# Kernel optimization log

Measured on AMD Instinct MI355X. Metric: run time of the kernel, lower is better.

The kernel has to match this reference:

```python
import jax, jax.numpy as jnp
import numpy as np

B, N, D, H, QK, HID = 4, 1024, 1024, 16, 64, 4096
BETA = 1.0 / float(np.sqrt(QK))  # default attn_beta = 1/sqrt(qk_dim)


def setup_inputs() -> dict:
    key = jax.random.key(0)
    k1, k2, k3, k4 = jax.random.split(key, 4)
    x = jax.random.normal(k1, (B, N, D), dtype=jnp.float32)
    scale = 1.0 / float(np.sqrt(D))
    Wq = jax.random.normal(k2, (H, QK, D), dtype=jnp.float32) * scale
    Wk = jax.random.normal(k3, (H, QK, D), dtype=jnp.float32) * scale
    W_hop = jax.random.normal(k4, (D, HID), dtype=jnp.float32) * scale
    return {"x": x, "Wq": Wq, "Wk": Wk, "W_hop": W_hop}


def _energy(x, Wq, Wk, W_hop):
    # Graph energy attention (dense path, no adjacency / mask)
    q = jnp.einsum('bnd,hqd->bhnq', x, Wq)  # [B,H,N,QK]
    k = jnp.einsum('bnd,hqd->bhnq', x, Wk)  # [B,H,N,QK]
    scores = BETA * jnp.einsum('bhnq,bhmq->bhnm', q, k)  # [B,H,N,N]
    e_attn = -(1.0 / BETA) * jnp.sum(jax.nn.logsumexp(scores, axis=-1))
    # Hopfield energy: -1/2 * sum relu(x W)^2
    h = jax.nn.relu(jnp.einsum('bnd,de->bne', x, W_hop))  # [B,N,HID]
    e_hop = -0.5 * jnp.sum(h * h)
    return e_attn + e_hop


def reference(x, Wq, Wk, W_hop):
    # Module returns (grad of energy w.r.t. x, energy) via grad_and_value
    energy, grad = jax.value_and_grad(_energy, argnums=0)(x, Wq, Wk, W_hop)
    return grad, energy
```

## Files before the change

### kernel.cpp

```cpp
#include <hip/hip_runtime.h>
#include <hip/hip_bf16.h>
#include <math.h>

#define BETA 0.125f
#define INV_BETA 8.0f

typedef __attribute__((ext_vector_type(8))) short short8v;
typedef __attribute__((ext_vector_type(4))) float f32x4;
typedef union { short8v v; unsigned short u[8]; } v8u;

#define OFF_XB   0u
#define OFF_WCB  2097152u
#define OFF_WCTB 3145728u
#define OFF_WHB  4194304u
#define OFF_WHTB 6291456u
#define OFF_H    8388608u
#define OFF_QB   16777216u
#define OFF_KB   18874368u
#define OFF_QT   20971520u
#define OFF_KT   23068672u
#define OFF_DQK  25165824u
#define OFF_LSE  29360128u
#define OFF_PL   29425664u
#define OFF_PH   29429760u

__device__ __forceinline__ unsigned short f2b(float f) {
    unsigned u = __float_as_uint(f);
    return (unsigned short)((u + 0x7fffu + ((u >> 16) & 1u)) >> 16);
}

__device__ __forceinline__ void gload_lds16(const unsigned short* g, void* l) {
    __builtin_amdgcn_global_load_lds(
        (const __attribute__((address_space(1))) unsigned int*)g,
        (__attribute__((address_space(3))) unsigned int*)l, 16, 0, 0);
}

__global__ __launch_bounds__(256) void k_castall(const float* __restrict__ x,
                                                 const float* __restrict__ Wq,
                                                 const float* __restrict__ Wk,
                                                 const float* __restrict__ Whop,
                                                 unsigned short* __restrict__ XB,
                                                 unsigned short* __restrict__ WCB,
                                                 unsigned short* __restrict__ WHB) {
    int i = blockIdx.x * 256 + threadIdx.x;
    const float* s;
    unsigned short* d;
    int j;
    if (i < 1048576) { s = x; d = XB; j = i; }
    else if (i < 1310720) { s = Wq; d = WCB; j = i - 1048576; }
    else if (i < 1572864) { s = Wk; d = WCB + 1048576; j = i - 1310720; }
    else { s = Whop; d = WHB; j = i - 1572864; }
    float4 v = ((const float4*)s)[j];
    ushort4 o;
    o.x = f2b(v.x); o.y = f2b(v.y); o.z = f2b(v.z); o.w = f2b(v.w);
    ((ushort4*)d)[j] = o;
}

__global__ void k_tall(const float* __restrict__ Wq, const float* __restrict__ Wk,
                       const float* __restrict__ Whop,
                       unsigned short* __restrict__ WCTB, unsigned short* __restrict__ WHTB) {
    __shared__ float t[32][33];
    int bx = blockIdx.x;
    int tx = threadIdx.x, ty = threadIdx.y;
    if (bx < 64) {
        int j0 = bx * 32, d0 = blockIdx.y * 32;
#pragma unroll
        for (int i = 0; i < 4; ++i) {
            int j = j0 + ty + 8 * i;
            const float* src = (j < 1024) ? (Wq + (size_t)j * 1024) : (Wk + (size_t)(j - 1024) * 1024);
            t[ty + 8 * i][tx] = src[d0 + tx];
        }
        __syncthreads();
#pragma unroll
        for (int i = 0; i < 4; ++i)
            WCTB[(size_t)(d0 + ty + 8 * i) * 2048 + j0 + tx] = f2b(t[tx][ty + 8 * i]);
    } else {
        int e0 = (bx - 64) * 32, d0 = blockIdx.y * 32;
#pragma unroll
        for (int i = 0; i < 4; ++i)
            t[ty + 8 * i][tx] = Whop[(size_t)(d0 + ty + 8 * i) * 4096 + e0 + tx];
        __syncthreads();
#pragma unroll
        for (int i = 0; i < 4; ++i)
            WHTB[(size_t)(e0 + ty + 8 * i) * 1024 + d0 + tx] = f2b(t[tx][ty + 8 * i]);
    }
}

template <int MI, int NJ>
__device__ __forceinline__ void gemm_core(const unsigned short* __restrict__ A, int lda,
                                          const unsigned short* __restrict__ Bm, int ldb,
                                          int kdim, int rowBase, int colBase,
                                          unsigned short* ldsA, unsigned short* ldsB,
                                          f32x4 (&acc)[MI][NJ]) {
    const int tid = threadIdx.x, lane = tid & 63;
    const int wv = tid >> 6;
    const int lr = lane & 15, lg = lane >> 4;
    const int wrow = (wv >> 1) * (MI * 16);
    const int wcol = (wv & 1) * (NJ * 16);

    for (int kk = 0; kk < kdim; kk += 64) {
#pragma unroll
        for (int iss = 0; iss < MI; ++iss) {
            int p = iss * 256 + tid;
            int row = p >> 3, c = p & 7, cs = c ^ (row & 7);
            gload_lds16(&A[(size_t)(rowBase + row) * lda + kk + cs * 8], (char*)ldsA + p * 16);
        }
#pragma unroll
        for (int iss = 0; iss < NJ; ++iss) {
            int p = iss * 256 + tid;
            int row = p >> 3, c = p & 7, cs = c ^ (row & 7);
            gload_lds16(&Bm[(size_t)(colBase + row) * ldb + kk + cs * 8], (char*)ldsB + p * 16);
        }
        __syncthreads();
#pragma unroll
        for (int kc = 0; kc < 2; ++kc) {
            short8v av[MI], bv[NJ];
#pragma unroll
            for (int i = 0; i < MI; ++i) {
                int row = wrow + i * 16 + lr;
                av[i] = *(const short8v*)((const char*)ldsA + row * 128 + ((kc * 4 + lg) ^ (row & 7)) * 16);
            }
#pragma unroll
            for (int j = 0; j < NJ; ++j) {
                int row = wcol + j * 16 + lr;
                bv[j] = *(const short8v*)((const char*)ldsB + row * 128 + ((kc * 4 + lg) ^ (row & 7)) * 16);
            }
#pragma unroll
            for (int i = 0; i < MI; ++i)
#pragma unroll
                for (int j = 0; j < NJ; ++j)
                    acc[i][j] = __builtin_amdgcn_mfma_f32_16x16x32_bf16(av[i], bv[j], acc[i][j], 0, 0, 0);
        }
        __syncthreads();
    }
}

#define GEMM_IDX(MI, NJ)                                                         \
    const int tid = threadIdx.x, lane = tid & 63, wv = tid >> 6;                 \
    const int lr = lane & 15, lg = lane >> 4;                                    \
    const int row0 = blockIdx.x * (MI * 32) + (wv >> 1) * (MI * 16);             \
    const int col0 = blockIdx.y * (NJ * 32) + (wv & 1) * (NJ * 16);              \
    f32x4 acc[MI][NJ];                                                           \
    _Pragma("unroll") for (int i = 0; i < MI; ++i)                               \
        _Pragma("unroll") for (int j = 0; j < NJ; ++j)                           \
            acc[i][j] = (f32x4){0.f, 0.f, 0.f, 0.f};

__global__ __launch_bounds__(256) void mm_proj(const unsigned short* __restrict__ XB,
                                               const unsigned short* __restrict__ WCB,
                                               unsigned short* __restrict__ Qb,
                                               unsigned short* __restrict__ Kb) {
    __shared__ unsigned short ldsA[64 * 64];
    __shared__ unsigned short ldsB[128 * 64];
    GEMM_IDX(2, 4)
    gemm_core<2, 4>(XB, 1024, WCB, 1024, 1024, blockIdx.x * 64, blockIdx.y * 128, ldsA, ldsB, acc);
    unsigned short* dst = (col0 < 1024) ? Qb : Kb;
    const int cbase = col0 & 1023;
#pragma unroll
    for (int i = 0; i < 2; ++i)
#pragma unroll
        for (int r = 0; r < 4; ++r) {
            int rg = row0 + i * 16 + lg * 4 + r;
            int bb = rg >> 10, n = rg & 1023;
#pragma unroll
            for (int j = 0; j < 4; ++j) {
                int c = cbase + j * 16 + lr;
                int h = c >> 6, q = c & 63;
                dst[((size_t)(bb * 16 + h) * 1024 + n) * 64 + q] = f2b(acc[i][j][r]);
            }
        }
}

__global__ __launch_bounds__(256) void mm_hopfwd(const unsigned short* __restrict__ XB,
                                                 const unsigned short* __restrict__ WHTB,
                                                 unsigned short* __restrict__ H,
                                                 float* __restrict__ PH) {
    __shared__ unsigned short ldsA[128 * 64];
    __shared__ unsigned short ldsB[128 * 64];
    __shared__ float red[4];
    GEMM_IDX(4, 4)
    gemm_core<4, 4>(XB, 1024, WHTB, 1024, 1024, blockIdx.x * 128, blockIdx.y * 128, ldsA, ldsB, acc);
    float ss = 0.f;
#pragma unroll
    for (int i = 0; i < 4; ++i)
#pragma unroll
        for (int r = 0; r < 4; ++r) {
            size_t rg = row0 + i * 16 + lg * 4 + r;
#pragma unroll
            for (int j = 0; j < 4; ++j) {
                float hv = fmaxf(acc[i][j][r], 0.f);
                ss += hv * hv;
                H[rg * 4096 + col0 + j * 16 + lr] = f2b(hv);
            }
        }
#pragma unroll
    for (int off = 32; off; off >>= 1) ss += __shfl_down(ss, off);
    if (lane == 0) red[wv] = ss;
    __syncthreads();
    if (tid == 0) PH[blockIdx.y * gridDim.x + blockIdx.x] = red[0] + red[1] + red[2] + red[3];
}

__global__ __launch_bounds__(256) void mm_hopbwd(const unsigned short* __restrict__ H,
                                                 const unsigned short* __restrict__ WHB,
                                                 float* __restrict__ out) {
    __shared__ unsigned short ldsA[64 * 64];
    __shared__ unsigned short ldsB[64 * 64];
    GEMM_IDX(2, 2)
    gemm_core<2, 2>(H, 4096, WHB, 4096, 4096, blockIdx.x * 64, blockIdx.y * 64, ldsA, ldsB, acc);
#pragma unroll
    for (int i = 0; i < 2; ++i)
#pragma unroll
        for (int r = 0; r < 4; ++r) {
            size_t rg = row0 + i * 16 + lg * 4 + r;
#pragma unroll
            for (int j = 0; j < 2; ++j)
                out[rg * 1024 + col0 + j * 16 + lr] = -acc[i][j][r];
        }
}

__global__ __launch_bounds__(256) void mm_gradproj(const unsigned short* __restrict__ DQK,
                                                   const unsigned short* __restrict__ WCTB,
                                                   float* __restrict__ out) {
    __shared__ unsigned short ldsA[64 * 64];
    __shared__ unsigned short ldsB[64 * 64];
    GEMM_IDX(2, 2)
    gemm_core<2, 2>(DQK, 2048, WCTB, 2048, 2048, blockIdx.x * 64, blockIdx.y * 64, ldsA, ldsB, acc);
#pragma unroll
    for (int i = 0; i < 2; ++i)
#pragma unroll
        for (int r = 0; r < 4; ++r) {
            size_t rg = row0 + i * 16 + lg * 4 + r;
#pragma unroll
            for (int j = 0; j < 2; ++j) {
                size_t idx = rg * 1024 + col0 + j * 16 + lr;
                out[idx] += acc[i][j][r];
            }
        }
}

__global__ __launch_bounds__(256) void k_tqk(const unsigned short* __restrict__ Qb,
                                             const unsigned short* __restrict__ Kb,
                                             unsigned short* __restrict__ QT,
                                             unsigned short* __restrict__ KT) {
    __shared__ unsigned short T[64][65];
    const int z = blockIdx.z;
    const unsigned short* src = z ? Kb : Qb;
    unsigned short* dst = z ? KT : QT;
    const int bh = blockIdx.y;
    const int n0 = blockIdx.x * 64;
    const int t = threadIdx.x;
    {
        int row = t >> 3;
        int colc = (t & 7) * 8;
#pragma unroll
        for (int ii = 0; ii < 2; ++ii) {
            int r = row + 32 * ii;
            v8u vv;
            vv.v = *(const short8v*)&src[((size_t)(bh << 10) + n0 + r) * 64 + colc];
#pragma unroll
            for (int j = 0; j < 8; ++j) T[r][colc + j] = vv.u[j];
        }
    }
    __syncthreads();
    {
        int q = t >> 2;
        int nc = (t & 3) * 16;
        unsigned short buf[16];
#pragma unroll
        for (int j = 0; j < 16; ++j) buf[j] = T[nc + j][q];
        *(short8v*)&dst[((size_t)bh * 64 + q) * 1024 + n0 + nc] = *(short8v*)&buf[0];
        *(short8v*)&dst[((size_t)bh * 64 + q) * 1024 + n0 + nc + 8] = *(short8v*)&buf[8];
    }
}

__global__ __launch_bounds__(256) void k_dq(const unsigned short* __restrict__ Qb,
                                            const unsigned short* __restrict__ Kb,
                                            const unsigned short* __restrict__ KT,
                                            float* __restrict__ LSE,
                                            float* __restrict__ PL,
                                            unsigned short* __restrict__ DQK) {
    __shared__ unsigned short Ktile[2][64 * 64];
    __shared__ unsigned short Ttile[2][64 * 64];
    __shared__ unsigned short P[4][1024];
    const int tid = threadIdx.x, lane = tid & 63, wv = tid >> 6;
    const int bh = blockIdx.x, nt = blockIdx.y;
    const int nw = nt * 64 + wv * 16;
    const int lr = lane & 15, lg = lane >> 4;
    unsigned short* Pw = &P[wv][0];

    auto stage = [&](int buf, int m0) {
#pragma unroll
        for (int iss = 0; iss < 2; ++iss) {
            int p = iss * 256 + tid;
            int row = p >> 3, c = p & 7, cs = c ^ (row & 7);
            gload_lds16(&Kb[((size_t)(bh << 10) + m0 + row) * 64 + cs * 8],
                        (char*)&Ktile[buf][0] + p * 16);
            gload_lds16(&KT[((size_t)bh * 64 + row) * 1024 + m0 + cs * 8],
                        (char*)&Ttile[buf][0] + p * 16);
        }
    };

    short8v qa[2];
#pragma unroll
    for (int kc = 0; kc < 2; ++kc)
        qa[kc] = *(const short8v*)&Qb[((size_t)(bh << 10) + nw + lr) * 64 + kc * 32 + lg * 8];

    float sm[4];
    f32x4 dq[4];
#pragma unroll
    for (int r = 0; r < 4; ++r) sm[r] = 0.f;
#pragma unroll
    for (int qb = 0; qb < 4; ++qb) dq[qb] = (f32x4){0.f, 0.f, 0.f, 0.f};

    stage(0, 0);
    __syncthreads();
    int buf = 0;
    for (int mt = 0; mt < 16; ++mt) {
        if (mt < 15) stage(buf ^ 1, (mt + 1) * 64);
        const char* Kt = (const char*)&Ktile[buf][0];
        const char* Tt = (const char*)&Ttile[buf][0];
#pragma unroll
        for (int ct = 0; ct < 4; ++ct) {
            int brow = ct * 16 + lr;
            short8v bk0 = *(const short8v*)(Kt + brow * 128 + ((lg) ^ (brow & 7)) * 16);
            short8v bk1 = *(const short8v*)(Kt + brow * 128 + ((lg + 4) ^ (brow & 7)) * 16);
            f32x4 s = {0.f, 0.f, 0.f, 0.f};
            s = __builtin_amdgcn_mfma_f32_16x16x32_bf16(qa[0], bk0, s, 0, 0, 0);
            s = __builtin_amdgcn_mfma_f32_16x16x32_bf16(qa[1], bk1, s, 0, 0, 0);
#pragma unroll
            for (int r = 0; r < 4; ++r) {
                float p = __expf(s[r] * BETA);
                sm[r] += p;
                int row = lg * 4 + r;
                int off = (row * 64 + ct * 16 + lr) ^ ((row & 7) << 3);
                Pw[off] = f2b(p);
            }
        }
        short8v pa[2];
#pragma unroll
        for (int kc = 0; kc < 2; ++kc) {
            int off = (lr * 64 + kc * 32 + lg * 8) ^ ((lr & 7) << 3);
            pa[kc] = *(const short8v*)&Pw[off];
        }
#pragma unroll
        for (int qb = 0; qb < 4; ++qb) {
            int brow = qb * 16 + lr;
            short8v b0 = *(const short8v*)(Tt + brow * 128 + ((lg) ^ (brow & 7)) * 16);
            short8v b1 = *(const short8v*)(Tt + brow * 128 + ((lg + 4) ^ (brow & 7)) * 16);
            dq[qb] = __builtin_amdgcn_mfma_f32_16x16x32_bf16(pa[0], b0, dq[qb], 0, 0, 0);
            dq[qb] = __builtin_amdgcn_mfma_f32_16x16x32_bf16(pa[1], b1, dq[qb], 0, 0, 0);
        }
        __syncthreads();
        buf ^= 1;
    }

#pragma unroll
    for (int off = 1; off < 16; off <<= 1)
#pragma unroll
        for (int r = 0; r < 4; ++r) sm[r] += __shfl_xor(sm[r], off);

    const int b = bh >> 4, h = bh & 15;
#pragma unroll
    for (int r = 0; r < 4; ++r) {
        float inv = 1.0f / sm[r];
#pragma unroll
        for (int qb = 0; qb < 4; ++qb)
            DQK[((size_t)(b << 10) + nw + lg * 4 + r) * 2048 + h * 64 + qb * 16 + lr] =
                f2b(-dq[qb][r] * inv);
    }

    float lsum = 0.f;
    if (lr == 0) {
#pragma unroll
        for (int r = 0; r < 4; ++r) {
            float l = __logf(sm[r]);
            LSE[(size_t)(bh << 10) + nw + lg * 4 + r] = l;
            lsum += l;
        }
    }
    lsum += __shfl_xor(lsum, 16);
    lsum += __shfl_xor(lsum, 32);
    if (lane == 0) PL[(size_t)(bh * 16 + nt) * 4 + wv] = lsum;
}

__global__ __launch_bounds__(256) void k_dk(const unsigned short* __restrict__ Qb,
                                            const unsigned short* __restrict__ Kb,
                                            const unsigned short* __restrict__ QT,
                                            const float* __restrict__ LSE,
                                            unsigned short* __restrict__ DQK) {
    __shared__ unsigned short Qtile[2][64 * 64];
    __shared__ unsigned short Ttile[2][64 * 64];
    __shared__ unsigned short P[4][1024];
    const int tid = threadIdx.x, lane = tid & 63, wv = tid >> 6;
    const int bh = blockIdx.x, mt = blockIdx.y;
    const int mw = mt * 64 + wv * 16;
    const int lr = lane & 15, lg = lane >> 4;
    unsigned short* Pw = &P[wv][0];

    auto stage = [&](int buf, int n0) {
#pragma unroll
        for (int iss = 0; iss < 2; ++iss) {
            int p = iss * 256 + tid;
            int row = p >> 3, c = p & 7, cs = c ^ (row & 7);
            gload_lds16(&Qb[((size_t)(bh << 10) + n0 + row) * 64 + cs * 8],
                        (char*)&Qtile[buf][0] + p * 16);
            gload_lds16(&QT[((size_t)bh * 64 + row) * 1024 + n0 + cs * 8],
                        (char*)&Ttile[buf][0] + p * 16);
        }
    };

    short8v ka[2];
#pragma unroll
    for (int kc = 0; kc < 2; ++kc)
        ka[kc] = *(const short8v*)&Kb[((size_t)(bh << 10) + mw + lr) * 64 + kc * 32 + lg * 8];

    f32x4 dk[4];
#pragma unroll
    for (int qb = 0; qb < 4; ++qb) dk[qb] = (f32x4){0.f, 0.f, 0.f, 0.f};

    stage(0, 0);
    __syncthreads();
    int buf = 0;
    for (int ntl = 0; ntl < 16; ++ntl) {
        const int n0 = ntl * 64;
        float lse_c[4];
#pragma unroll
        for (int ct = 0; ct < 4; ++ct)
            lse_c[ct] = LSE[(size_t)(bh << 10) + n0 + ct * 16 + lr];
        if (ntl < 15) stage(buf ^ 1, n0 + 64);
        const char* Qt = (const char*)&Qtile[buf][0];
        const char* Tt = (const char*)&Ttile[buf][0];
#pragma unroll
        for (int ct = 0; ct < 4; ++ct) {
            int brow = ct * 16 + lr;
            short8v bq0 = *(const short8v*)(Qt + brow * 128 + ((lg) ^ (brow & 7)) * 16);
            short8v bq1 = *(const short8v*)(Qt + brow * 128 + ((lg + 4) ^ (brow & 7)) * 16);
            f32x4 s = {0.f, 0.f, 0.f, 0.f};
            s = __builtin_amdgcn_mfma_f32_16x16x32_bf16(ka[0], bq0, s, 0, 0, 0);
            s = __builtin_amdgcn_mfma_f32_16x16x32_bf16(ka[1], bq1, s, 0, 0, 0);
#pragma unroll
            for (int r = 0; r < 4; ++r) {
                float p = __expf(s[r] * BETA - lse_c[ct]);
                int row = lg * 4 + r;
                int off = (row * 64 + ct * 16 + lr) ^ ((row & 7) << 3);
                Pw[off] = f2b(p);
            }
        }
        short8v pa[2];
#pragma unroll
        for (int kc = 0; kc < 2; ++kc) {
            int off = (lr * 64 + kc * 32 + lg * 8) ^ ((lr & 7) << 3);
            pa[kc] = *(const short8v*)&Pw[off];
        }
#pragma unroll
        for (int qb = 0; qb < 4; ++qb) {
            int brow = qb * 16 + lr;
            short8v b0 = *(const short8v*)(Tt + brow * 128 + ((lg) ^ (brow & 7)) * 16);
            short8v b1 = *(const short8v*)(Tt + brow * 128 + ((lg + 4) ^ (brow & 7)) * 16);
            dk[qb] = __builtin_amdgcn_mfma_f32_16x16x32_bf16(pa[0], b0, dk[qb], 0, 0, 0);
            dk[qb] = __builtin_amdgcn_mfma_f32_16x16x32_bf16(pa[1], b1, dk[qb], 0, 0, 0);
        }
        __syncthreads();
        buf ^= 1;
    }
    const int b = bh >> 4, h = bh & 15;
#pragma unroll
    for (int qb = 0; qb < 4; ++qb)
#pragma unroll
        for (int r = 0; r < 4; ++r)
            DQK[((size_t)(b << 10) + mw + lg * 4 + r) * 2048 + 1024 + h * 64 + qb * 16 + lr] = f2b(-dk[qb][r]);
}

__global__ __launch_bounds__(256) void k_fin(const float* __restrict__ pl,
                                             const float* __restrict__ ph,
                                             float* __restrict__ out) {
    const int tid = threadIdx.x;
    float s1 = 0.f, s2 = 0.f;
    for (int i = tid; i < 4096; i += 256) s1 += pl[i];
    for (int i = tid; i < 1024; i += 256) s2 += ph[i];
#pragma unroll
    for (int off = 32; off; off >>= 1) {
        s1 += __shfl_down(s1, off);
        s2 += __shfl_down(s2, off);
    }
    __shared__ float r1[4], r2[4];
    if ((tid & 63) == 0) { r1[tid >> 6] = s1; r2[tid >> 6] = s2; }
    __syncthreads();
    if (tid == 0) {
        float S1 = r1[0] + r1[1] + r1[2] + r1[3];
        float S2 = r2[0] + r2[1] + r2[2] + r2[3];
        out[(size_t)4194304] = -INV_BETA * S1 - 0.5f * S2;
    }
}

extern "C" void kernel_launch(void* const* d_in, const int* in_sizes, int n_in,
                              void* d_out, int out_size, void* d_ws, size_t ws_size,
                              hipStream_t stream) {
    (void)in_sizes; (void)n_in; (void)out_size; (void)ws_size;
    const float* x    = (const float*)d_in[0];
    const float* Wq   = (const float*)d_in[1];
    const float* Wk   = (const float*)d_in[2];
    const float* Whop = (const float*)d_in[3];
    float* out = (float*)d_out;
    float* ws = (float*)d_ws;

    unsigned short* XB   = (unsigned short*)(ws + OFF_XB);
    unsigned short* WCB  = (unsigned short*)(ws + OFF_WCB);
    unsigned short* WCTB = (unsigned short*)(ws + OFF_WCTB);
    unsigned short* WHB  = (unsigned short*)(ws + OFF_WHB);
    unsigned short* WHTB = (unsigned short*)(ws + OFF_WHTB);
    unsigned short* H    = (unsigned short*)(ws + OFF_H);
    unsigned short* Qb   = (unsigned short*)(ws + OFF_QB);
    unsigned short* Kb   = (unsigned short*)(ws + OFF_KB);
    unsigned short* QT   = (unsigned short*)(ws + OFF_QT);
    unsigned short* KT   = (unsigned short*)(ws + OFF_KT);
    unsigned short* DQK  = (unsigned short*)(ws + OFF_DQK);
    float* LSE = ws + OFF_LSE;
    float* PL  = ws + OFF_PL;
    float* PH  = ws + OFF_PH;

    dim3 blk(256);
    k_castall<<<dim3(10240), blk, 0, stream>>>(x, Wq, Wk, Whop, XB, WCB, WHB);
    k_tall<<<dim3(192, 32), dim3(32, 8), 0, stream>>>(Wq, Wk, Whop, WCTB, WHTB);

    mm_proj<<<dim3(64, 16), blk, 0, stream>>>(XB, WCB, Qb, Kb);
    k_tqk<<<dim3(16, 64, 2), blk, 0, stream>>>(Qb, Kb, QT, KT);
    k_dq<<<dim3(64, 16), blk, 0, stream>>>(Qb, Kb, KT, LSE, PL, DQK);
    k_dk<<<dim3(64, 16), blk, 0, stream>>>(Qb, Kb, QT, LSE, DQK);

    mm_hopfwd<<<dim3(32, 32), blk, 0, stream>>>(XB, WHTB, H, PH);
    mm_hopbwd<<<dim3(64, 16), blk, 0, stream>>>(H, WHB, out);
    mm_gradproj<<<dim3(64, 16), blk, 0, stream>>>(DQK, WCTB, out);
    k_fin<<<dim3(1), blk, 0, stream>>>(PL, PH, out);
}
```

Baseline: 330.2 us.

## Fuse Hopfield and projection gradient GEMMs and add XCD-aware block swizzle

Merges the Hopfield backward GEMM and the Q/K gradient projection GEMM into one kernel that accumulates both K-loops into the same registers and writes the output once. The ReLU activations are stored negated, so the sign flip moves out of the epilogue and the read-modify-write of the output goes away. Grids are flattened to 1D with a swizzle that groups neighbouring tiles onto the same XCD, aiming for better L2 reuse. This adds one fewer launch and removes a full fp32 output round trip, at the cost of a longer-running fused kernel.

After: 330.0 us. No clear change (-0.0%).

```diff
diff --git a/kernel.cpp b/kernel.cpp
--- a/kernel.cpp
+++ b/kernel.cpp
@@ -33,6 +33,13 @@
     __builtin_amdgcn_global_load_lds(
         (const __attribute__((address_space(1))) unsigned int*)g,
         (__attribute__((address_space(3))) unsigned int*)l, 16, 0, 0);
+}
+
+__device__ __forceinline__ void xcd_swz(int n, int gx, int& bx, int& by) {
+    int id = blockIdx.x;
+    int nid = (id & 7) * (n >> 3) + (id >> 3);
+    bx = nid % gx;
+    by = nid / gx;
 }
 
 __global__ __launch_bounds__(256) void k_castall(const float* __restrict__ x,
@@ -135,11 +142,11 @@
     }
 }
 
-#define GEMM_IDX(MI, NJ)                                                         \
+#define GEMM_IDX(MI, NJ, BX, BY)                                                 \
     const int tid = threadIdx.x, lane = tid & 63, wv = tid >> 6;                 \
     const int lr = lane & 15, lg = lane >> 4;                                    \
-    const int row0 = blockIdx.x * (MI * 32) + (wv >> 1) * (MI * 16);             \
-    const int col0 = blockIdx.y * (NJ * 32) + (wv & 1) * (NJ * 16);              \
+    const int row0 = (BX) * (MI * 32) + (wv >> 1) * (MI * 16);                   \
+    const int col0 = (BY) * (NJ * 32) + (wv & 1) * (NJ * 16);                    \
     f32x4 acc[MI][NJ];                                                           \
     _Pragma("unroll") for (int i = 0; i < MI; ++i)                               \
         _Pragma("unroll") for (int j = 0; j < NJ; ++j)                           \
@@ -151,8 +158,10 @@
                                                unsigned short* __restrict__ Kb) {
     __shared__ unsigned short ldsA[64 * 64];
     __shared__ unsigned short ldsB[128 * 64];
-    GEMM_IDX(2, 4)
-    gemm_core<2, 4>(XB, 1024, WCB, 1024, 1024, blockIdx.x * 64, blockIdx.y * 128, ldsA, ldsB, acc);
+    int bx, by;
+    xcd_swz(1024, 64, bx, by);
+    GEMM_IDX(2, 4, bx, by)
+    gemm_core<2, 4>(XB, 1024, WCB, 1024, 1024, bx * 64, by * 128, ldsA, ldsB, acc);
     unsigned short* dst = (col0 < 1024) ? Qb : Kb;
     const int cbase = col0 & 1023;
 #pragma unroll
@@ -172,13 +181,15 @@
 
 __global__ __launch_bounds__(256) void mm_hopfwd(const unsigned short* __restrict__ XB,
                                                  const unsigned short* __restrict__ WHTB,
-                                                 unsigned short* __restrict__ H,
+                                                 unsigned short* __restrict__ Hn,
                                                  float* __restrict__ PH) {
     __shared__ unsigned short ldsA[128 * 64];
     __shared__ unsigned short ldsB[128 * 64];
     __shared__ float red[4];
-    GEMM_IDX(4, 4)
-    gemm_core<4, 4>(XB, 1024, WHTB, 1024, 1024, blockIdx.x * 128, blockIdx.y * 128, ldsA, ldsB, acc);
+    int bx, by;
+    xcd_swz(1024, 32, bx, by);
+    GEMM_IDX(4, 4, bx, by)
+    gemm_core<4, 4>(XB, 1024, WHTB, 1024, 1024, bx * 128, by * 128, ldsA, ldsB, acc);
     float ss = 0.f;
 #pragma unroll
     for (int i = 0; i < 4; ++i)
@@ -189,23 +200,28 @@
             for (int j = 0; j < 4; ++j) {
                 float hv = fmaxf(acc[i][j][r], 0.f);
                 ss += hv * hv;
-                H[rg * 4096 + col0 + j * 16 + lr] = f2b(hv);
+                Hn[rg * 4096 + col0 + j * 16 + lr] = f2b(-hv);
             }
         }
 #pragma unroll
     for (int off = 32; off; off >>= 1) ss += __shfl_down(ss, off);
     if (lane == 0) red[wv] = ss;
     __syncthreads();
-    if (tid == 0) PH[blockIdx.y * gridDim.x + blockIdx.x] = red[0] + red[1] + red[2] + red[3];
-}
-
-__global__ __launch_bounds__(256) void mm_hopbwd(const unsigned short* __restrict__ H,
-                                                 const unsigned short* __restrict__ WHB,
-                                                 float* __restrict__ out) {
+    if (tid == 0) PH[blockIdx.x] = red[0] + red[1] + red[2] + red[3];
+}
+
+__global__ __launch_bounds__(256) void mm_gradall(const unsigned short* __restrict__ Hn,
+                                                  const unsigned short* __restrict__ WHB,
+                                                  const unsigned short* __restrict__ DQK,
+                                                  const unsigned short* __restrict__ WCTB,
+                                                  float* __restrict__ out) {
     __shared__ unsigned short ldsA[64 * 64];
     __shared__ unsigned short ldsB[64 * 64];
-    GEMM_IDX(2, 2)
-    gemm_core<2, 2>(H, 4096, WHB, 4096, 4096, blockIdx.x * 64, blockIdx.y * 64, ldsA, ldsB, acc);
+    int bx, by;
+    xcd_swz(1024, 64, bx, by);
+    GEMM_IDX(2, 2, bx, by)
+    gemm_core<2, 2>(Hn, 4096, WHB, 4096, 4096, bx * 64, by * 64, ldsA, ldsB, acc);
+    gemm_core<2, 2>(DQK, 2048, WCTB, 2048, 2048, bx * 64, by * 64, ldsA, ldsB, acc);
 #pragma unroll
     for (int i = 0; i < 2; ++i)
 #pragma unroll
@@ -213,27 +229,7 @@
             size_t rg = row0 + i * 16 + lg * 4 + r;
 #pragma unroll
             for (int j = 0; j < 2; ++j)
-                out[rg * 1024 + col0 + j * 16 + lr] = -acc[i][j][r];
-        }
-}
-
-__global__ __launch_bounds__(256) void mm_gradproj(const unsigned short* __restrict__ DQK,
-                                                   const unsigned short* __restrict__ WCTB,
-                                                   float* __restrict__ out) {
-    __shared__ unsigned short ldsA[64 * 64];
-    __shared__ unsigned short ldsB[64 * 64];
-    GEMM_IDX(2, 2)
-    gemm_core<2, 2>(DQK, 2048, WCTB, 2048, 2048, blockIdx.x * 64, blockIdx.y * 64, ldsA, ldsB, acc);
-#pragma unroll
-    for (int i = 0; i < 2; ++i)
-#pragma unroll
-        for (int r = 0; r < 4; ++r) {
-            size_t rg = row0 + i * 16 + lg * 4 + r;
-#pragma unroll
-            for (int j = 0; j < 2; ++j) {
-                size_t idx = rg * 1024 + col0 + j * 16 + lr;
-                out[idx] += acc[i][j][r];
-            }
+                out[rg * 1024 + col0 + j * 16 + lr] = acc[i][j][r];
         }
 }
 
@@ -281,8 +277,9 @@
     __shared__ unsigned short Ktile[2][64 * 64];
     __shared__ unsigned short Ttile[2][64 * 64];
     __shared__ unsigned short P[4][1024];
+    int nt, bh;
+    xcd_swz(1024, 16, nt, bh);
     const int tid = threadIdx.x, lane = tid & 63, wv = tid >> 6;
-    const int bh = blockIdx.x, nt = blockIdx.y;
     const int nw = nt * 64 + wv * 16;
     const int lr = lane & 15, lg = lane >> 4;
     unsigned short* Pw = &P[wv][0];
@@ -379,7 +376,7 @@
     }
     lsum += __shfl_xor(lsum, 16);
     lsum += __shfl_xor(lsum, 32);
-    if (lane == 0) PL[(size_t)(bh * 16 + nt) * 4 + wv] = lsum;
+    if (lane == 0) PL[(size_t)blockIdx.x * 4 + wv] = lsum;
 }
 
 __global__ __launch_bounds__(256) void k_dk(const unsigned short* __restrict__ Qb,
@@ -390,8 +387,9 @@
     __shared__ unsigned short Qtile[2][64 * 64];
     __shared__ unsigned short Ttile[2][64 * 64];
     __shared__ unsigned short P[4][1024];
+    int mt, bh;
+    xcd_swz(1024, 16, mt, bh);
     const int tid = threadIdx.x, lane = tid & 63, wv = tid >> 6;
-    const int bh = blockIdx.x, mt = blockIdx.y;
     const int mw = mt * 64 + wv * 16;
     const int lr = lane & 15, lg = lane >> 4;
     unsigned short* Pw = &P[wv][0];
@@ -508,7 +506,7 @@
     unsigned short* WCTB = (unsigned short*)(ws + OFF_WCTB);
     unsigned short* WHB  = (unsigned short*)(ws + OFF_WHB);
     unsigned short* WHTB = (unsigned short*)(ws + OFF_WHTB);
-    unsigned short* H    = (unsigned short*)(ws + OFF_H);
+    unsigned short* Hn   = (unsigned short*)(ws + OFF_H);
     unsigned short* Qb   = (unsigned short*)(ws + OFF_QB);
     unsigned short* Kb   = (unsigned short*)(ws + OFF_KB);
     unsigned short* QT   = (unsigned short*)(ws + OFF_QT);
@@ -522,13 +520,12 @@
     k_castall<<<dim3(10240), blk, 0, stream>>>(x, Wq, Wk, Whop, XB, WCB, WHB);
     k_tall<<<dim3(192, 32), dim3(32, 8), 0, stream>>>(Wq, Wk, Whop, WCTB, WHTB);
 
-    mm_proj<<<dim3(64, 16), blk, 0, stream>>>(XB, WCB, Qb, Kb);
+    mm_proj<<<dim3(1024), blk, 0, stream>>>(XB, WCB, Qb, Kb);
     k_tqk<<<dim3(16, 64, 2), blk, 0, stream>>>(Qb, Kb, QT, KT);
-    k_dq<<<dim3(64, 16), blk, 0, stream>>>(Qb, Kb, KT, LSE, PL, DQK);
-    k_dk<<<dim3(64, 16), blk, 0, stream>>>(Qb, Kb, QT, LSE, DQK);
-
-    mm_hopfwd<<<dim3(32, 32), blk, 0, stream>>>(XB, WHTB, H, PH);
-    mm_hopbwd<<<dim3(64, 16), blk, 0, stream>>>(H, WHB, out);
-    mm_gradproj<<<dim3(64, 16), blk, 0, stream>>>(DQK, WCTB, out);
+    k_dq<<<dim3(1024), blk, 0, stream>>>(Qb, Kb, KT, LSE, PL, DQK);
+    k_dk<<<dim3(1024), blk, 0, stream>>>(Qb, Kb, QT, LSE, DQK);
+
+    mm_hopfwd<<<dim3(1024), blk, 0, stream>>>(XB, WHTB, Hn, PH);
+    mm_gradall<<<dim3(1024), blk, 0, stream>>>(Hn, WHB, DQK, WCTB, out);
     k_fin<<<dim3(1), blk, 0, stream>>>(PL, PH, out);
 }
```
